# Kernel tuning notes

Hardware: AMD Instinct MI355X
Metric: run time of the kernel (lower is better)

## Reference

```python
import jax, jax.numpy as jnp
import numpy as np

V, E, HID, K, S = 100000, 256, 512, 20, 4096
HD = HID // 2  # per-direction LSTM hidden
START_ID, STOP_ID = 18, 19


def setup_inputs() -> dict:
    key = jax.random.key(0)
    ks = jax.random.split(key, 14)
    sentence = jax.random.randint(ks[0], (S,), 0, V)
    tags = jax.random.randint(ks[1], (S,), 0, START_ID)  # real tags only
    embed = jax.random.normal(ks[2], (V, E), jnp.float32) * 0.1
    w_ih_f = jax.random.normal(ks[3], (4 * HD, E), jnp.float32) * 0.05
    w_hh_f = jax.random.normal(ks[4], (4 * HD, HD), jnp.float32) * 0.05
    b_f = jax.random.normal(ks[5], (4 * HD,), jnp.float32) * 0.05
    w_ih_b = jax.random.normal(ks[6], (4 * HD, E), jnp.float32) * 0.05
    w_hh_b = jax.random.normal(ks[7], (4 * HD, HD), jnp.float32) * 0.05
    b_b = jax.random.normal(ks[8], (4 * HD,), jnp.float32) * 0.05
    h0 = jax.random.normal(ks[9], (2, HD), jnp.float32)
    c0 = jax.random.normal(ks[10], (2, HD), jnp.float32)
    emit_W = jax.random.normal(ks[11], (K, HID), jnp.float32) * 0.05
    emit_b = jax.random.normal(ks[12], (K,), jnp.float32) * 0.05
    transition = jax.random.normal(ks[13], (K, K), jnp.float32)
    transition = transition.at[START_ID, :].set(-10000.0)
    transition = transition.at[:, STOP_ID].set(-10000.0)
    return dict(sentence=sentence, tags=tags, embed=embed,
                w_ih_f=w_ih_f, w_hh_f=w_hh_f, b_f=b_f,
                w_ih_b=w_ih_b, w_hh_b=w_hh_b, b_b=b_b,
                h0=h0, c0=c0, emit_W=emit_W, emit_b=emit_b,
                transition=transition)


def _lstm_scan(xs, w_ih, w_hh, b, h, c):
    # xs: (S, E); torch gate order i, f, g, o
    def step(carry, x):
        h, c = carry
        z = x @ w_ih.T + h @ w_hh.T + b  # (4*HD,)
        i, f, g, o = jnp.split(z, 4)
        i, f, o = jax.nn.sigmoid(i), jax.nn.sigmoid(f), jax.nn.sigmoid(o)
        g = jnp.tanh(g)
        c = f * c + i * g
        h = o * jnp.tanh(c)
        return (h, c), h
    _, hs = jax.lax.scan(step, (h, c), xs)
    return hs  # (S, HD)


def reference(sentence, tags, embed, w_ih_f, w_hh_f, b_f,
              w_ih_b, w_hh_b, b_b, h0, c0, emit_W, emit_b, transition):
    xs = embed[sentence]  # (S, E)
    h_fwd = _lstm_scan(xs, w_ih_f, w_hh_f, b_f, h0[0], c0[0])
    h_bwd = _lstm_scan(xs[::-1], w_ih_b, w_hh_b, b_b, h0[1], c0[1])[::-1]
    feats = jnp.concatenate([h_fwd, h_bwd], axis=-1) @ emit_W.T + emit_b  # (S, K)

    # CRF forward algorithm (log-partition), tag dim fully vectorized.
    init_fv = jnp.full((K,), -10000.0, feats.dtype).at[START_ID].set(0.0)

    def crf_step(fv, feat):
        # fv_new[next] = logsumexp_prev(fv[prev] + T[next, prev] + feat[next])
        fv = jax.scipy.special.logsumexp(fv[None, :] + transition + feat[:, None], axis=1)
        return fv, None

    fv, _ = jax.lax.scan(crf_step, init_fv, feats)
    log_z = jax.scipy.special.logsumexp(fv + transition[STOP_ID])

    # Gold path score.
    tags_ext = jnp.concatenate([jnp.array([START_ID], tags.dtype), tags])
    gold = (transition[tags_ext[1:], tags_ext[:-1]].sum()
            + feats[jnp.arange(S), tags].sum()
            + transition[STOP_ID, tags[-1]])
    return jnp.stack([log_z, gold])
```

## Files before the change

kernel.cpp:

```cpp
#include <hip/hip_runtime.h>
#include <stdint.h>

#define SLEN 4096
#define EDIM 256
#define HD 256
#define G4 1024
#define KT 20
#define START_ID 18
#define STOP_ID 19

typedef _Float16 half_t;
typedef _Float16 half2_t __attribute__((ext_vector_type(2)));

__device__ __forceinline__ float dot2(uint32_t w, uint32_t h, float acc) {
#if __has_builtin(__builtin_amdgcn_fdot2)
    return __builtin_amdgcn_fdot2(__builtin_bit_cast(half2_t, w),
                                  __builtin_bit_cast(half2_t, h), acc, false);
#else
    half2_t wv = __builtin_bit_cast(half2_t, w);
    half2_t hv = __builtin_bit_cast(half2_t, h);
    acc += (float)wv.x * (float)hv.x;
    acc += (float)wv.y * (float)hv.y;
    return acc;
#endif
}

__device__ __forceinline__ float fsig(float x) { return 1.f / (1.f + __expf(-x)); }
__device__ __forceinline__ float ftanh(float x) { return 1.f - 2.f / (__expf(2.f * x) + 1.f); }


__global__ __launch_bounds__(256) void k_transpose_ih(const float* __restrict__ wf,
                                                      const float* __restrict__ wb,
                                                      float* __restrict__ wT) {
    __shared__ float tile[32][33];
    int d = blockIdx.z;
    const float* w = d ? wb : wf;
    int ob = blockIdx.x * 32;
    int eb = blockIdx.y * 32;
    int tx = threadIdx.x & 31, ty = threadIdx.x >> 5;
#pragma unroll
    for (int r = 0; r < 32; r += 8)
        tile[ty + r][tx] = w[(long)(ob + ty + r) * EDIM + eb + tx];
    __syncthreads();
    float* dst = wT + (long)d * EDIM * G4;
#pragma unroll
    for (int r = 0; r < 32; r += 8)
        dst[(long)(eb + ty + r) * G4 + ob + tx] = tile[tx][ty + r];
}

__global__ __launch_bounds__(1024) void k_pack_hh(const float* __restrict__ whf,
                                                  const float* __restrict__ whb,
                                                  uint4* __restrict__ wpack,
                                                  uint32_t* __restrict__ flags) {
    int b = blockIdx.x;
    int d = b >> 1, half = b & 1;
    const float* W = d ? whb : whf;
    int t = threadIdx.x;
    int l = t & 63, w = t >> 6;
    int ju = ((w & 7) << 4) | (l & 15);
    int kq = ((w >> 3) << 2) | (l >> 4);
    if (b == 0 && t < 4) flags[t] = 0;
#pragma unroll
    for (int cc = 0; cc < 16; cc++) {
        int g = cc >> 2, kc = cc & 3;
        int row = g * 256 + half * 128 + ju;
        int kb = kq * 32 + kc * 8;
        uint32_t q[4];
#pragma unroll
        for (int dw = 0; dw < 4; dw++) {
            half2_t p = {(half_t)W[(long)row * HD + kb + 2 * dw],
                         (half_t)W[(long)row * HD + kb + 2 * dw + 1]};
            q[dw] = __builtin_bit_cast(uint32_t, p);
        }
        wpack[(b * 16 + cc) * 1024 + t] = make_uint4(q[0], q[1], q[2], q[3]);
    }
}

__global__ __launch_bounds__(256) void k_zx(const int* __restrict__ sentence,
                                            const float* __restrict__ embed,
                                            const float* __restrict__ wT,
                                            const float* __restrict__ bf,
                                            const float* __restrict__ bb,
                                            float* __restrict__ zxp) {
    int d = blockIdx.y;
    int s0 = blockIdx.x * 16;
    const float* bias = d ? bb : bf;
    __shared__ float xbuf[16][EDIM];
    int u = threadIdx.x;
    for (int r = 0; r < 16; r++) {
        int row = sentence[s0 + r];
        xbuf[r][u] = embed[(long)row * EDIM + u];
    }
    __syncthreads();
    const float* wTd = wT + (long)d * EDIM * G4;
    float4 a[16];
    float4 bv = make_float4(bias[u], bias[256 + u], bias[512 + u], bias[768 + u]);
#pragma unroll
    for (int r = 0; r < 16; r++) a[r] = bv;
    for (int e = 0; e < EDIM; e += 4) {
        float w0[4], w1[4], w2[4], w3[4];
#pragma unroll
        for (int k = 0; k < 4; k++) {
            w0[k] = wTd[(long)(e + k) * G4 + u];
            w1[k] = wTd[(long)(e + k) * G4 + 256 + u];
            w2[k] = wTd[(long)(e + k) * G4 + 512 + u];
            w3[k] = wTd[(long)(e + k) * G4 + 768 + u];
        }
#pragma unroll
        for (int r = 0; r < 16; r++) {
            float4 x4 = *(const float4*)&xbuf[r][e];
            float xv[4] = {x4.x, x4.y, x4.z, x4.w};
#pragma unroll
            for (int k = 0; k < 4; k++) {
                a[r].x += w0[k] * xv[k];
                a[r].y += w1[k] * xv[k];
                a[r].z += w2[k] * xv[k];
                a[r].w += w3[k] * xv[k];
            }
        }
    }
#pragma unroll
    for (int r = 0; r < 16; r++)
        *(float4*)&zxp[(long)(d * SLEN + s0 + r) * G4 + u * 4] = a[r];
}

__global__ __launch_bounds__(1024, 4) void k_lstm(const float* __restrict__ zxp,
                                                  const uint4* __restrict__ wpack,
                                                  const float* __restrict__ h0,
                                                  const float* __restrict__ c0,
                                                  float* __restrict__ hs,
                                                  uint32_t* __restrict__ hx,
                                                  uint32_t* __restrict__ flags) {
    __shared__ __align__(16) half_t hfull[256];
    __shared__ __align__(16) half_t hown[2][128];
    __shared__ __align__(16) float zpart[128][4];

    int b = blockIdx.x, d = b >> 1, half = b & 1;
    int t = threadIdx.x, l = t & 63, w = t >> 6;
    int kqg = w >> 3;
    bool ownw = (kqg == half);
    int ju = ((w & 7) << 4) | (l & 15);
    int j = (half << 7) | ju;
    int kq = (kqg << 2) | (l >> 4);

    const uint4* wpd = wpack + (long)(b << 4) * 1024;
    uint4 wreg[16];
#pragma unroll
    for (int cc = 0; cc < 16; cc++) wreg[cc] = wpd[cc * 1024 + t];

    float c = c0[d * HD + j];
    if (t < 128) {
        half2_t p0 = {(half_t)h0[d * HD + 2 * t], (half_t)h0[d * HD + 2 * t + 1]};
        ((uint32_t*)hfull)[t] = __builtin_bit_cast(uint32_t, p0);
    }
    __syncthreads();

    const float* zxd = zxp + (long)d * SLEN * G4;
    float* hsd = hs + (long)d * SLEN * HD + j;
    uint32_t* hx_mine = hx + b * 128;
    const uint32_t* hx_part = hx + (b ^ 1) * 128;
    uint32_t* mflag = flags + b;
    uint32_t* pflag = flags + (b ^ 1);
    const int pubw = half ? 7 : 15;

    float4 zxn = make_float4(0.f, 0.f, 0.f, 0.f);
    if (ownw) zxn = *(const float4*)&zxd[(long)(d ? SLEN - 1 : 0) * G4 + j * 4];

    for (int s = 0; s < SLEN; s++) {
        const int p = s & 1;
        float4 zxq = zxn;
        if (ownw && s + 1 < SLEN) {
            int sxn = d ? (SLEN - 2 - s) : (s + 1);
            zxn = *(const float4*)&zxd[(long)sxn * G4 + j * 4];
        }

        uint4 hv0, hv1, hv2, hv3;
        if (s == 0) {
            const char* hb = (const char*)hfull + (kq << 6);
            hv0 = *(const uint4*)(hb);      hv1 = *(const uint4*)(hb + 16);
            hv2 = *(const uint4*)(hb + 32); hv3 = *(const uint4*)(hb + 48);
        } else if (ownw) {
            const char* hb = (const char*)hown + p * 256 + ((l >> 4) << 6);
            hv0 = *(const uint4*)(hb);      hv1 = *(const uint4*)(hb + 16);
            hv2 = *(const uint4*)(hb + 32); hv3 = *(const uint4*)(hb + 48);
        } else {
            const uint32_t tgt = (uint32_t)s;
            while (__hip_atomic_load(pflag, __ATOMIC_RELAXED, __HIP_MEMORY_SCOPE_AGENT) < tgt)
                __builtin_amdgcn_s_sleep(2);
            asm volatile("" ::: "memory");
            const uint32_t* src = hx_part + p * 64 + ((l >> 4) << 4);
            uint32_t hw[16];
#pragma unroll
            for (int q2 = 0; q2 < 16; q2++)
                hw[q2] = __hip_atomic_load(src + q2, __ATOMIC_RELAXED, __HIP_MEMORY_SCOPE_AGENT);
            hv0 = make_uint4(hw[0], hw[1], hw[2], hw[3]);
            hv1 = make_uint4(hw[4], hw[5], hw[6], hw[7]);
            hv2 = make_uint4(hw[8], hw[9], hw[10], hw[11]);
            hv3 = make_uint4(hw[12], hw[13], hw[14], hw[15]);
        }

        float a0 = 0.f, b0 = 0.f, a1 = 0.f, b1 = 0.f;
        float a2 = 0.f, b2 = 0.f, a3 = 0.f, b3 = 0.f;
#define DOT4(kc, HV)                                                      \
        a0 = dot2(wreg[kc].x, HV.x, a0);      b0 = dot2(wreg[kc].y, HV.y, b0);      \
        a0 = dot2(wreg[kc].z, HV.z, a0);      b0 = dot2(wreg[kc].w, HV.w, b0);      \
        a1 = dot2(wreg[4 + kc].x, HV.x, a1);  b1 = dot2(wreg[4 + kc].y, HV.y, b1);  \
        a1 = dot2(wreg[4 + kc].z, HV.z, a1);  b1 = dot2(wreg[4 + kc].w, HV.w, b1);  \
        a2 = dot2(wreg[8 + kc].x, HV.x, a2);  b2 = dot2(wreg[8 + kc].y, HV.y, b2);  \
        a2 = dot2(wreg[8 + kc].z, HV.z, a2);  b2 = dot2(wreg[8 + kc].w, HV.w, b2);  \
        a3 = dot2(wreg[12 + kc].x, HV.x, a3); b3 = dot2(wreg[12 + kc].y, HV.y, b3); \
        a3 = dot2(wreg[12 + kc].z, HV.z, a3); b3 = dot2(wreg[12 + kc].w, HV.w, b3);
        DOT4(0, hv0)
        DOT4(1, hv1)
        DOT4(2, hv2)
        DOT4(3, hv3)
#undef DOT4
        float zi = a0 + b0, zf = a1 + b1, zg = a2 + b2, zo = a3 + b3;
        zi += __shfl_xor(zi, 16, 64);
        zf += __shfl_xor(zf, 16, 64);
        zg += __shfl_xor(zg, 16, 64);
        zo += __shfl_xor(zo, 16, 64);
        zi += __shfl_xor(zi, 32, 64);
        zf += __shfl_xor(zf, 32, 64);
        zg += __shfl_xor(zg, 32, 64);
        zo += __shfl_xor(zo, 32, 64);

        if (!ownw && (l >> 4) == 0)
            *(float4*)&zpart[ju][0] = make_float4(zi, zf, zg, zo);
        __syncthreads();

        if (ownw) {
            float4 zp = *(const float4*)&zpart[ju][0];
            float Zi = zi + zp.x + zxq.x;
            float Zf = zf + zp.y + zxq.y;
            float Zg = zg + zp.z + zxq.z;
            float Zo = zo + zp.w + zxq.w;
            float ig = fsig(Zi), fg = fsig(Zf), og = fsig(Zo);
            float gg = ftanh(Zg);
            c = fg * c + ig * gg;
            float hval = og * ftanh(c);
            if ((l >> 4) == 0) {
                int sx = d ? (SLEN - 1 - s) : s;
                hsd[(long)sx * HD] = hval;
                hown[p ^ 1][ju] = (half_t)hval;
            }
        }
        __syncthreads();

        if (w == pubw && s + 1 < SLEN) {
            if (l < 16) {
                uint4 v = *(const uint4*)((const char*)hown + (p ^ 1) * 256 + l * 16);
                *(uint4*)(hx_mine + (p ^ 1) * 64 + l * 4) = v;
            }
            __threadfence();
            if (l == 0)
                __hip_atomic_store(mflag, (uint32_t)(s + 1), __ATOMIC_RELEASE,
                                   __HIP_MEMORY_SCOPE_AGENT);
        }
    }
}

__global__ __launch_bounds__(192) void k_feats(const float* __restrict__ hs,
                                               const float* __restrict__ emitW,
                                               const float* __restrict__ emitb,
                                               float* __restrict__ feats) {
    __shared__ float wb[KT][516];
    __shared__ float hb[8][516];
    int tid = threadIdx.x;
    int s0 = blockIdx.x * 8;
    for (int idx = tid; idx < KT * 512; idx += 192) {
        wb[idx >> 9][idx & 511] = emitW[idx];
    }
    for (int idx = tid; idx < 8 * 512; idx += 192) {
        int sl = idx >> 9, jj = idx & 511;
        float v = (jj < 256) ? hs[(long)(s0 + sl) * HD + jj]
                             : hs[(long)(SLEN + s0 + sl) * HD + (jj - 256)];
        hb[sl][jj] = v;
    }
    __syncthreads();
    if (tid < 160) {
        int sl = tid / KT, k = tid % KT;
        float acc = emitb[k];
        for (int jj = 0; jj < 512; jj += 4) {
            float4 wv = *(const float4*)&wb[k][jj];
            float4 hv = *(const float4*)&hb[sl][jj];
            acc += wv.x * hv.x + wv.y * hv.y + wv.z * hv.z + wv.w * hv.w;
        }
        feats[(long)(s0 + sl) * KT + k] = acc;
    }
}

__global__ __launch_bounds__(256) void k_gold(const float* __restrict__ feats,
                                              const int* __restrict__ tags,
                                              const float* __restrict__ trans,
                                              float* __restrict__ out) {
    __shared__ float red[256];
    int tid = threadIdx.x;
    float local = 0.f;
    for (int s2 = tid; s2 < SLEN; s2 += 256) {
        int cur = tags[s2];
        int prev = s2 ? tags[s2 - 1] : START_ID;
        local += trans[cur * KT + prev] + feats[(long)s2 * KT + cur];
    }
    red[tid] = local;
    __syncthreads();
    for (int off = 128; off; off >>= 1) {
        if (tid < off) red[tid] += red[tid + off];
        __syncthreads();
    }
    if (tid == 0) out[1] = red[0] + trans[STOP_ID * KT + tags[SLEN - 1]];
}

__global__ __launch_bounds__(512) void k_crf_chunk(const float* __restrict__ feats,
                                                   const float* __restrict__ trans,
                                                   float* __restrict__ mats) {
    __shared__ float T[KT][KT + 1];
    __shared__ float fb[16][KT];
    __shared__ float cur[2][KT][KT + 1];
    int tid = threadIdx.x;
    int t0 = blockIdx.x * 16;
    if (tid < KT * KT) T[tid / KT][tid % KT] = trans[tid];
    for (int idx = tid; idx < 16 * KT; idx += 512) fb[idx / KT][idx % KT] = feats[(long)t0 * KT + idx];
    __syncthreads();
    int i = tid / KT, jc = tid % KT;
    bool act = tid < KT * KT;
    if (act) cur[0][i][jc] = T[i][jc] + fb[0][i];
    __syncthreads();
    for (int m = 1; m < 16; m++) {
        int p = (m - 1) & 1;
        float nv = 0.f;
        if (act) {
            float vs[KT], vmax = -1e30f;
#pragma unroll
            for (int k = 0; k < KT; k++) { vs[k] = T[i][k] + cur[p][k][jc]; vmax = fmaxf(vmax, vs[k]); }
            float sum = 0.f;
#pragma unroll
            for (int k = 0; k < KT; k++) sum += __expf(vs[k] - vmax);
            nv = fb[m][i] + vmax + __logf(sum);
        }
        if (act) cur[p ^ 1][i][jc] = nv;
        __syncthreads();
    }
    if (act) mats[(long)blockIdx.x * (KT * KT) + tid] = cur[1][i][jc];
}

__global__ __launch_bounds__(512) void k_crf_combine(const float* __restrict__ in,
                                                     float* __restrict__ out_mats,
                                                     int per_block,
                                                     const float* __restrict__ trans,
                                                     float* __restrict__ d_out_ptr,
                                                     int finalize) {
    __shared__ float A[KT][KT + 1];
    __shared__ float cur[2][KT][KT + 1];
    int tid = threadIdx.x;
    int b = blockIdx.x;
    int i = tid / KT, jc = tid % KT;
    bool act = tid < KT * KT;
    const float* base = in + (long)b * per_block * (KT * KT);
    if (act) cur[0][i][jc] = base[tid];
    __syncthreads();
    for (int m = 1; m < per_block; m++) {
        int p = (m - 1) & 1;
        if (act) A[i][jc] = base[(long)m * KT * KT + tid];
        __syncthreads();
        float nv = 0.f;
        if (act) {
            float vs[KT], vmax = -1e30f;
#pragma unroll
            for (int k = 0; k < KT; k++) { vs[k] = A[i][k] + cur[p][k][jc]; vmax = fmaxf(vmax, vs[k]); }
            float sum = 0.f;
#pragma unroll
            for (int k = 0; k < KT; k++) sum += __expf(vs[k] - vmax);
            nv = vmax + __logf(sum);
        }
        if (act) cur[p ^ 1][i][jc] = nv;
        __syncthreads();
    }
    int fbuf = (per_block - 1) & 1;
    if (!finalize) {
        if (act) out_mats[(long)b * KT * KT + tid] = cur[fbuf][i][jc];
        return;
    }
    if (tid == 0) {
        float fv[KT];
        for (int ii = 0; ii < KT; ii++) {
            float vs[KT], vmax = -1e30f;
            for (int k = 0; k < KT; k++) {
                float v = cur[fbuf][ii][k] + (k == START_ID ? 0.f : -10000.f);
                vs[k] = v;
                vmax = fmaxf(vmax, v);
            }
            float sum = 0.f;
            for (int k = 0; k < KT; k++) sum += __expf(vs[k] - vmax);
            fv[ii] = vmax + __logf(sum);
        }
        float vs2[KT], vmax = -1e30f;
        for (int ii = 0; ii < KT; ii++) {
            float v = fv[ii] + trans[STOP_ID * KT + ii];
            vs2[ii] = v;
            vmax = fmaxf(vmax, v);
        }
        float sum = 0.f;
        for (int ii = 0; ii < KT; ii++) sum += __expf(vs2[ii] - vmax);
        d_out_ptr[0] = vmax + __logf(sum);
    }
}

extern "C" void kernel_launch(void* const* d_in, const int* in_sizes, int n_in,
                              void* d_out, int out_size, void* d_ws, size_t ws_size,
                              hipStream_t stream) {
    const int* sentence = (const int*)d_in[0];
    const int* tags = (const int*)d_in[1];
    const float* embed = (const float*)d_in[2];
    const float* w_ih_f = (const float*)d_in[3];
    const float* w_hh_f = (const float*)d_in[4];
    const float* b_f = (const float*)d_in[5];
    const float* w_ih_b = (const float*)d_in[6];
    const float* w_hh_b = (const float*)d_in[7];
    const float* b_b = (const float*)d_in[8];
    const float* h0 = (const float*)d_in[9];
    const float* c0 = (const float*)d_in[10];
    const float* emit_W = (const float*)d_in[11];
    const float* emit_b = (const float*)d_in[12];
    const float* transition = (const float*)d_in[13];
    float* out = (float*)d_out;

    char* ws = (char*)d_ws;
    float* zxp = (float*)(ws + 0);
    float* hs = (float*)(ws + 33554432);
    float* wT = (float*)(ws + 41943040);
    uint4* wpack = (uint4*)(ws + 44040192);
    float* feats = (float*)(ws + 45088768);
    float* mats = (float*)(ws + 45416448);
    float* mats2 = (float*)(ws + 45826048);
    uint32_t* hx = (uint32_t*)(ws + 45851648);
    uint32_t* flags = (uint32_t*)(ws + 45855744);

    k_transpose_ih<<<dim3(32, 8, 2), 256, 0, stream>>>(w_ih_f, w_ih_b, wT);
    k_pack_hh<<<dim3(4), 1024, 0, stream>>>(w_hh_f, w_hh_b, wpack, flags);
    k_zx<<<dim3(256, 2), 256, 0, stream>>>(sentence, embed, wT, b_f, b_b, zxp);
    k_lstm<<<dim3(4), 1024, 0, stream>>>(zxp, wpack, h0, c0, hs, hx, flags);
    k_feats<<<dim3(512), 192, 0, stream>>>(hs, emit_W, emit_b, feats);
    k_gold<<<dim3(1), 256, 0, stream>>>(feats, tags, transition, out);
    k_crf_chunk<<<dim3(256), 512, 0, stream>>>(feats, transition, mats);
    k_crf_combine<<<dim3(16), 512, 0, stream>>>(mats, mats2, 16, transition, out, 0);
    k_crf_combine<<<dim3(1), 512, 0, stream>>>(mats2, nullptr, 16, transition, out, 1);
}
```

Baseline: 9.001 ms.

## Replace flag-and-fence handshake with step-tagged hidden-state words in LSTM exchange

```diff
diff --git a/kernel.cpp b/kernel.cpp
--- a/kernel.cpp
+++ b/kernel.cpp
@@ -50,8 +50,7 @@
 
 __global__ __launch_bounds__(1024) void k_pack_hh(const float* __restrict__ whf,
                                                   const float* __restrict__ whb,
-                                                  uint4* __restrict__ wpack,
-                                                  uint32_t* __restrict__ flags) {
+                                                  uint4* __restrict__ wpack) {
     int b = blockIdx.x;
     int d = b >> 1, half = b & 1;
     const float* W = d ? whb : whf;
@@ -59,7 +58,6 @@
     int l = t & 63, w = t >> 6;
     int ju = ((w & 7) << 4) | (l & 15);
     int kq = ((w >> 3) << 2) | (l >> 4);
-    if (b == 0 && t < 4) flags[t] = 0;
 #pragma unroll
     for (int cc = 0; cc < 16; cc++) {
         int g = cc >> 2, kc = cc & 3;
@@ -129,8 +127,7 @@
                                                   const float* __restrict__ h0,
                                                   const float* __restrict__ c0,
                                                   float* __restrict__ hs,
-                                                  uint32_t* __restrict__ hx,
-                                                  uint32_t* __restrict__ flags) {
+                                                  uint32_t* __restrict__ hx) {
     __shared__ __align__(16) half_t hfull[256];
     __shared__ __align__(16) half_t hown[2][128];
     __shared__ __align__(16) float zpart[128][4];
@@ -157,11 +154,8 @@
 
     const float* zxd = zxp + (long)d * SLEN * G4;
     float* hsd = hs + (long)d * SLEN * HD + j;
-    uint32_t* hx_mine = hx + b * 128;
-    const uint32_t* hx_part = hx + (b ^ 1) * 128;
-    uint32_t* mflag = flags + b;
-    uint32_t* pflag = flags + (b ^ 1);
-    const int pubw = half ? 7 : 15;
+    uint32_t* hx_mine = hx + b * 256;
+    const uint32_t* hx_part = hx + (b ^ 1) * 256;
 
     float4 zxn = make_float4(0.f, 0.f, 0.f, 0.f);
     if (ownw) zxn = *(const float4*)&zxd[(long)(d ? SLEN - 1 : 0) * G4 + j * 4];
@@ -184,19 +178,29 @@
             hv0 = *(const uint4*)(hb);      hv1 = *(const uint4*)(hb + 16);
             hv2 = *(const uint4*)(hb + 32); hv3 = *(const uint4*)(hb + 48);
         } else {
-            const uint32_t tgt = (uint32_t)s;
-            while (__hip_atomic_load(pflag, __ATOMIC_RELAXED, __HIP_MEMORY_SCOPE_AGENT) < tgt)
-                __builtin_amdgcn_s_sleep(2);
-            asm volatile("" ::: "memory");
-            const uint32_t* src = hx_part + p * 64 + ((l >> 4) << 4);
-            uint32_t hw[16];
+            const uint32_t* src = hx_part + (p << 7) + ((l >> 4) << 5);
+            const uint32_t want = (uint32_t)s;
+            uint32_t hw[32];
+            int iters = 0;
+            for (;;) {
+#pragma unroll
+                for (int q2 = 0; q2 < 32; q2++)
+                    hw[q2] = __hip_atomic_load(src + q2, __ATOMIC_RELAXED,
+                                               __HIP_MEMORY_SCOPE_AGENT);
+                uint32_t agg = 0;
+#pragma unroll
+                for (int q2 = 0; q2 < 32; q2++) agg |= (hw[q2] >> 16) ^ want;
+                if (agg == 0) break;
+                if (++iters > (1 << 22)) break;
+            }
+            uint32_t hp[16];
 #pragma unroll
             for (int q2 = 0; q2 < 16; q2++)
-                hw[q2] = __hip_atomic_load(src + q2, __ATOMIC_RELAXED, __HIP_MEMORY_SCOPE_AGENT);
-            hv0 = make_uint4(hw[0], hw[1], hw[2], hw[3]);
-            hv1 = make_uint4(hw[4], hw[5], hw[6], hw[7]);
-            hv2 = make_uint4(hw[8], hw[9], hw[10], hw[11]);
-            hv3 = make_uint4(hw[12], hw[13], hw[14], hw[15]);
+                hp[q2] = (hw[2 * q2] & 0xFFFFu) | (hw[2 * q2 + 1] << 16);
+            hv0 = make_uint4(hp[0], hp[1], hp[2], hp[3]);
+            hv1 = make_uint4(hp[4], hp[5], hp[6], hp[7]);
+            hv2 = make_uint4(hp[8], hp[9], hp[10], hp[11]);
+            hv3 = make_uint4(hp[12], hp[13], hp[14], hp[15]);
         }
 
         float a0 = 0.f, b0 = 0.f, a1 = 0.f, b1 = 0.f;
@@ -241,22 +245,18 @@
             float hval = og * ftanh(c);
             if ((l >> 4) == 0) {
                 int sx = d ? (SLEN - 1 - s) : s;
+                half_t hh = (half_t)hval;
                 hsd[(long)sx * HD] = hval;
-                hown[p ^ 1][ju] = (half_t)hval;
+                hown[p ^ 1][ju] = hh;
+                if (s + 1 < SLEN) {
+                    uint32_t word = ((uint32_t)(s + 1) << 16) |
+                                    (uint32_t)__builtin_bit_cast(uint16_t, hh);
+                    __hip_atomic_store(&hx_mine[(((s + 1) & 1) << 7) + ju], word,
+                                       __ATOMIC_RELAXED, __HIP_MEMORY_SCOPE_AGENT);
+                }
             }
         }
         __syncthreads();
-
-        if (w == pubw && s + 1 < SLEN) {
-            if (l < 16) {
-                uint4 v = *(const uint4*)((const char*)hown + (p ^ 1) * 256 + l * 16);
-                *(uint4*)(hx_mine + (p ^ 1) * 64 + l * 4) = v;
-            }
-            __threadfence();
-            if (l == 0)
-                __hip_atomic_store(mflag, (uint32_t)(s + 1), __ATOMIC_RELEASE,
-                                   __HIP_MEMORY_SCOPE_AGENT);
-        }
     }
 }
 
@@ -434,12 +434,11 @@
     float* mats = (float*)(ws + 45416448);
     float* mats2 = (float*)(ws + 45826048);
     uint32_t* hx = (uint32_t*)(ws + 45851648);
-    uint32_t* flags = (uint32_t*)(ws + 45855744);
 
     k_transpose_ih<<<dim3(32, 8, 2), 256, 0, stream>>>(w_ih_f, w_ih_b, wT);
-    k_pack_hh<<<dim3(4), 1024, 0, stream>>>(w_hh_f, w_hh_b, wpack, flags);
+    k_pack_hh<<<dim3(4), 1024, 0, stream>>>(w_hh_f, w_hh_b, wpack);
     k_zx<<<dim3(256, 2), 256, 0, stream>>>(sentence, embed, wT, b_f, b_b, zxp);
-    k_lstm<<<dim3(4), 1024, 0, stream>>>(zxp, wpack, h0, c0, hs, hx, flags);
+    k_lstm<<<dim3(4), 1024, 0, stream>>>(zxp, wpack, h0, c0, hs, hx);
     k_feats<<<dim3(512), 192, 0, stream>>>(hs, emit_W, emit_b, feats);
     k_gold<<<dim3(1), 256, 0, stream>>>(feats, tags, transition, out);
     k_crf_chunk<<<dim3(256), 512, 0, stream>>>(feats, transition, mats);
```

Measured after the change: 10.63 ms. 1.18x slower.
